# Optimization experiments

Measured on AMD Instinct MI355X. Metric: run time of the kernel, lower is better.

The kernel has to match this reference:

```python
import jax, jax.numpy as jnp
import numpy as np


def _forgetting_attn(q, k, v, g):
    # q, k, v: [B, T, H, D]; g: [B, T, H] per-step log decay (log-space)
    scale = q.shape[-1] ** -0.5
    scores = jnp.einsum('bqhd,bkhd->bhqk', q, k) * scale  # [B,H,T,T]
    gc = jnp.cumsum(g, axis=1).transpose(0, 2, 1)  # [B,H,T]
    scores = scores + gc[:, :, :, None] - gc[:, :, None, :]
    T = q.shape[1]
    causal = jnp.tril(jnp.ones((T, T), dtype=bool))
    scores = jnp.where(causal, scores, -jnp.inf)
    probs = jax.nn.softmax(scores.astype(jnp.float32), axis=-1).astype(q.dtype)
    return jnp.einsum('bhqk,bkhd->bqhd', probs, v)  # [B,T,H,D]


def setup_inputs() -> dict:
    key = jax.random.key(0)
    ks = jax.random.split(key, 7)
    B, T, H = 1, 2048, 1024
    nh = 16
    s = 0.02
    return {
        'hidden_states': jax.random.normal(ks[0], (B, T, H), jnp.float32),
        'Wq': jax.random.normal(ks[1], (H, H), jnp.float32) * s,
        'Wk': jax.random.normal(ks[2], (H, H), jnp.float32) * s,
        'Wv': jax.random.normal(ks[3], (H, H), jnp.float32) * s,
        'Wf': jax.random.normal(ks[4], (nh, H), jnp.float32) * s,
        'bf': jnp.zeros((nh,), jnp.float32),
        'Wo': jax.random.normal(ks[5], (H, 2 * H), jnp.float32) * s,
    }


def reference(hidden_states, Wq, Wk, Wv, Wf, bf, Wo):
    B, T, H = hidden_states.shape
    nh = Wf.shape[0]
    d = H // nh
    q = (hidden_states @ Wq.T).reshape(B, T, nh, d)
    k = (hidden_states @ Wk.T).reshape(B, T, nh, d)
    v = (hidden_states @ Wv.T).reshape(B, T, nh, d)
    f = jax.nn.log_sigmoid((hidden_states @ Wf.T + bf).astype(jnp.float32))  # [B,T,nh]
    o_fwd = _forgetting_attn(q, k, v, f)
    flip = lambda x: jnp.flip(x, axis=1)
    o_bwd = flip(_forgetting_attn(flip(q), flip(k), flip(v), flip(f)))
    o = jnp.concatenate([o_fwd.reshape(B, T, H), o_bwd.reshape(B, T, H)], axis=-1)
    return o @ Wo.T
```

## Files before the change

kernel.cpp:

```cpp
#include <hip/hip_runtime.h>
#include <math.h>

#define T_SEQ 2048
#define HID   1024
#define NH    16
#define HD    64
#define NT    (T_SEQ / 64)

typedef __attribute__((ext_vector_type(8))) __bf16 bf16x8;
typedef __attribute__((ext_vector_type(4))) float  f32x4;
typedef __attribute__((ext_vector_type(8))) unsigned short u16x8;

#define GPTR(p) (const __attribute__((address_space(1))) void*)(p)
#define SPTR(p) (__attribute__((address_space(3))) void*)(p)

__device__ __forceinline__ unsigned short f2bf(float x) {
    unsigned u = __float_as_uint(x);
    u = (u + 0x7FFF + ((u >> 16) & 1)) >> 16;
    return (unsigned short)u;
}
__device__ __forceinline__ float bf2f(unsigned short u) {
    return __uint_as_float((unsigned)u << 16);
}

__global__ __launch_bounds__(256) void prep1(
    const float* __restrict__ hs,
    const float* __restrict__ Wq, const float* __restrict__ Wk,
    const float* __restrict__ Wv, const float* __restrict__ Wo,
    const float* __restrict__ Wf, const float* __restrict__ bfv,
    unsigned short* __restrict__ hsb, unsigned short* __restrict__ wqb,
    unsigned short* __restrict__ wkb, unsigned short* __restrict__ wvb,
    unsigned short* __restrict__ wob, float* __restrict__ f)
{
    const int y = blockIdx.y;
    if (y < 5) {
        const float* in; unsigned short* out; int n;
        switch (y) {
            case 0: in = hs; out = hsb; n = T_SEQ * HID; break;
            case 1: in = Wq; out = wqb; n = HID * HID;   break;
            case 2: in = Wk; out = wkb; n = HID * HID;   break;
            case 3: in = Wv; out = wvb; n = HID * HID;   break;
            default: in = Wo; out = wob; n = HID * 2 * HID; break;
        }
        const int stride = gridDim.x * blockDim.x;
        for (int i = blockIdx.x * blockDim.x + threadIdx.x; i < n / 4; i += stride) {
            float4 v = reinterpret_cast<const float4*>(in)[i];
            ushort4 r;
            r.x = f2bf(v.x); r.y = f2bf(v.y); r.z = f2bf(v.z); r.w = f2bf(v.w);
            reinterpret_cast<ushort4*>(out)[i] = r;
        }
    } else {
        const int t  = blockIdx.x;
        const int h  = threadIdx.x >> 4;
        const int sl = threadIdx.x & 15;
        const float4* hrow = reinterpret_cast<const float4*>(hs + (size_t)t * HID);
        const float4* wrow = reinterpret_cast<const float4*>(Wf + (size_t)h * HID);
        float s = 0.f;
        #pragma unroll
        for (int i = 0; i < 16; ++i) {
            float4 a = hrow[sl + i * 16];
            float4 b = wrow[sl + i * 16];
            s += a.x * b.x + a.y * b.y + a.z * b.z + a.w * b.w;
        }
        s += __shfl_xor(s, 1);
        s += __shfl_xor(s, 2);
        s += __shfl_xor(s, 4);
        s += __shfl_xor(s, 8);
        if (sl == 0) {
            float x = s + bfv[h];
            f[t * NH + h] = (x >= 0.f) ? -log1pf(expf(-x)) : (x - log1pf(expf(x)));
        }
    }
}

template<int NCH, int ROWB>
__device__ __forceinline__ void stage_tile(const unsigned short* __restrict__ G, int K,
                                           int k0, unsigned short* lds, int tid, int w)
{
    #pragma unroll
    for (int j = 0; j < NCH; ++j) {
        const int idxb = j * 4096 + tid * 16;
        const int row  = idxb / ROWB;
        const int kbyt = idxb % ROWB;
        const int col  = (kbyt ^ ((row & 7) << 4)) >> 1;
        const int ldsh = (j * 4096 + w * 1024) >> 1;
        __builtin_amdgcn_global_load_lds(
            GPTR(G + (size_t)row * K + k0 + col), SPTR(lds + ldsh), 16, 0, 0);
    }
}

template<int BM, int BN, int BK, int EMODE>
__global__ __launch_bounds__(256) void gemm_mfma_bt(
    const unsigned short* __restrict__ A,
    const unsigned short* __restrict__ W0, const unsigned short* __restrict__ W1,
    const unsigned short* __restrict__ W2,
    float* __restrict__ C,
    unsigned short* __restrict__ qb, unsigned short* __restrict__ kb,
    unsigned short* __restrict__ vt,
    int M, int N, int K)
{
    const unsigned short* W = blockIdx.z == 0 ? W0 : (blockIdx.z == 1 ? W1 : W2);

    constexpr int FM   = BM / 32;
    constexpr int FN   = BN / 32;
    constexpr int ROWB = BK * 2;
    constexpr int NCHA = BM * BK * 2 / 4096;
    constexpr int NCHB = BN * BK * 2 / 4096;
    constexpr int NKS  = BK / 32;

    __shared__ unsigned short Als[2][BM * BK];
    __shared__ unsigned short Bls[2][BN * BK];

    const int gx  = gridDim.x;
    const int nwg = gx * gridDim.y;
    const int lin = blockIdx.y * gx + blockIdx.x;
    const int cpx = nwg >> 3;
    const int sw  = (lin & 7) * cpx + (lin >> 3);
    const int bx  = sw % gx;
    const int by  = sw / gx;

    const int tid = threadIdx.x;
    const int w   = tid >> 6;
    const int l   = tid & 63;
    const int bm  = by * BM;
    const int bn  = bx * BN;
    const int wm  = (w >> 1) * (BM / 2);
    const int wn  = (w & 1) * (BN / 2);

    f32x4 acc[FM][FN];
    #pragma unroll
    for (int m = 0; m < FM; ++m)
        #pragma unroll
        for (int n = 0; n < FN; ++n) acc[m][n] = (f32x4){0.f, 0.f, 0.f, 0.f};

    const int frow = l & 15;
    const int kgrp = (l >> 4) * 16;
    const int swz  = (l & 7) << 4;

    const unsigned short* Ag = A + (size_t)bm * K;
    const unsigned short* Wg = W + (size_t)bn * K;

    const int NIT = K / BK;
    stage_tile<NCHA, ROWB>(Ag, K, 0, Als[0], tid, w);
    stage_tile<NCHB, ROWB>(Wg, K, 0, Bls[0], tid, w);
    __syncthreads();

    int cur = 0;
    for (int it = 0; it < NIT; ++it) {
        if (it + 1 < NIT) {
            stage_tile<NCHA, ROWB>(Ag, K, (it + 1) * BK, Als[cur ^ 1], tid, w);
            stage_tile<NCHB, ROWB>(Wg, K, (it + 1) * BK, Bls[cur ^ 1], tid, w);
        }
        const unsigned short* Ap = Als[cur];
        const unsigned short* Bp = Bls[cur];
        #pragma unroll
        for (int ks = 0; ks < NKS; ++ks) {
            bf16x8 af[FM], bfr[FN];
            #pragma unroll
            for (int m = 0; m < FM; ++m) {
                const int off = (wm + m * 16 + frow) * ROWB + ((ks * 64 + kgrp) ^ swz);
                af[m] = *reinterpret_cast<const bf16x8*>((const char*)Ap + off);
            }
            #pragma unroll
            for (int n = 0; n < FN; ++n) {
                const int off = (wn + n * 16 + frow) * ROWB + ((ks * 64 + kgrp) ^ swz);
                bfr[n] = *reinterpret_cast<const bf16x8*>((const char*)Bp + off);
            }
            #pragma unroll
            for (int m = 0; m < FM; ++m)
                #pragma unroll
                for (int n = 0; n < FN; ++n)
                    acc[m][n] = __builtin_amdgcn_mfma_f32_16x16x32_bf16(
                        af[m], bfr[n], acc[m][n], 0, 0, 0);
        }
        __syncthreads();
        cur ^= 1;
    }

    const int r0 = (l >> 4) * 4;
    const int cc = l & 15;
    if (EMODE == 1) {
        #pragma unroll
        for (int m = 0; m < FM; ++m)
            #pragma unroll
            for (int n = 0; n < FN; ++n) {
                float* cp = C + (size_t)(bm + wm + m * 16 + r0) * N + bn + wn + n * 16 + cc;
                #pragma unroll
                for (int r = 0; r < 4; ++r) cp[(size_t)r * N] = acc[m][n][r];
            }
    } else {
        const int z = blockIdx.z;
        if (z == 0) {
            #pragma unroll
            for (int m = 0; m < FM; ++m) {
                const int t0 = bm + wm + m * 16 + r0;
                #pragma unroll
                for (int n = 0; n < FN; ++n) {
                    const int col = bn + wn + n * 16 + cc;
                    #pragma unroll
                    for (int r = 0; r < 4; ++r)
                        qb[(size_t)(t0 + r) * HID + col] = f2bf(acc[m][n][r] * 0.125f);
                }
            }
        } else if (z == 1) {
            #pragma unroll
            for (int m = 0; m < FM; ++m) {
                const int t0 = bm + wm + m * 16 + r0;
                #pragma unroll
                for (int n = 0; n < FN; ++n) {
                    const int col = bn + wn + n * 16 + cc;
                    const int hh  = col >> 6;
                    const int d   = col & 63;
                    #pragma unroll
                    for (int r = 0; r < 4; ++r)
                        kb[(size_t)hh * T_SEQ * HD + (size_t)(t0 + r) * HD + d] =
                            f2bf(acc[m][n][r]);
                }
            }
        } else {
            #pragma unroll
            for (int m = 0; m < FM; ++m) {
                const int t0 = bm + wm + m * 16 + r0;
                #pragma unroll
                for (int n = 0; n < FN; ++n) {
                    const int col = bn + wn + n * 16 + cc;
                    const int hh  = col >> 6;
                    const int d   = col & 63;
                    ushort4 pk;
                    pk.x = f2bf(acc[m][n][0]); pk.y = f2bf(acc[m][n][1]);
                    pk.z = f2bf(acc[m][n][2]); pk.w = f2bf(acc[m][n][3]);
                    *reinterpret_cast<ushort4*>(
                        vt + (size_t)hh * HD * T_SEQ + (size_t)d * T_SEQ + t0) = pk;
                }
            }
        }
    }
}

__global__ __launch_bounds__(256) void prep2(const float* __restrict__ f,
                                             float* __restrict__ gcf,
                                             float* __restrict__ gcb,
                                             const unsigned short* __restrict__ kb,
                                             float* __restrict__ knmax)
{
    const int bid = blockIdx.x;
    if (bid < 32) {
        const int h   = bid >> 1;
        const int rev = bid & 1;
        float* out = rev ? gcb : gcf;
        const int wv   = threadIdx.x >> 6;
        const int lane = threadIdx.x & 63;
        __shared__ float wtot[4];
        float vals[8];
        float run = 0.f;
        #pragma unroll
        for (int c = 0; c < 8; ++c) {
            const int p = wv * 512 + c * 64 + lane;
            const int t = rev ? (T_SEQ - 1 - p) : p;
            float x = f[t * NH + h];
            #pragma unroll
            for (int off = 1; off < 64; off <<= 1) {
                float y = __shfl_up(x, off);
                if (lane >= off) x += y;
            }
            vals[c] = run + x;
            run += __shfl(x, 63);
        }
        if (lane == 0) wtot[wv] = run;
        __syncthreads();
        float prefix = 0.f;
        #pragma unroll
        for (int i = 0; i < 4; ++i) prefix += (i < wv) ? wtot[i] : 0.f;
        #pragma unroll
        for (int c = 0; c < 8; ++c) {
            const int p = wv * 512 + c * 64 + lane;
            const int t = rev ? (T_SEQ - 1 - p) : p;
            out[t * NH + h] = vals[c] + prefix;
        }
    } else {
        const int h    = bid - 32;
        const int tid  = threadIdx.x;
        const int wv   = tid >> 6;
        const int lane = tid & 63;
        __shared__ float wmax[4];
        float mx = 0.f;
        for (int t = tid; t < T_SEQ; t += 256) {
            const u16x8* kr = reinterpret_cast<const u16x8*>(
                kb + (size_t)h * T_SEQ * HD + (size_t)t * HD);
            float s = 0.f;
            #pragma unroll
            for (int i = 0; i < 8; ++i) {
                u16x8 v8 = kr[i];
                #pragma unroll
                for (int j = 0; j < 8; ++j) { float x = bf2f(v8[j]); s += x * x; }
            }
            mx = fmaxf(mx, s);
        }
        #pragma unroll
        for (int off = 32; off > 0; off >>= 1) mx = fmaxf(mx, __shfl_xor(mx, off));
        if (lane == 0) wmax[wv] = mx;
        __syncthreads();
        if (tid == 0) {
            float m = fmaxf(fmaxf(wmax[0], wmax[1]), fmaxf(wmax[2], wmax[3]));
            knmax[h] = sqrtf(m);
        }
    }
}

__global__ __launch_bounds__(256) void attn_flash(
    const unsigned short* __restrict__ qb, const unsigned short* __restrict__ kg,
    const unsigned short* __restrict__ vg,
    const float* __restrict__ gcf, const float* __restrict__ gcb,
    const float* __restrict__ knmax,
    unsigned short* __restrict__ ocat)
{
    const int dir = blockIdx.z;
    const float* gc = dir ? gcb : gcf;
    const int h   = blockIdx.y;
    const int qt  = blockIdx.x;
    const int q0  = qt * 64;
    const int tid = threadIdx.x;
    const int w   = tid >> 6;
    const int l   = tid & 63;
    const int lm  = l & 15;
    const int lg  = l >> 4;
    const int swz = (l & 7) << 4;

    __shared__ unsigned short Kls[64 * 64];
    __shared__ unsigned short Vls[64 * 64];
    __shared__ unsigned short Pls[64 * 64];
    __shared__ float gks[64];
    __shared__ float qbs[64];

    const size_t kgbase = (size_t)h * T_SEQ * HD;
    const size_t vgbase = (size_t)h * HD * T_SEQ;

    const int qrow_a = q0 + 16 * w + lm;
    bf16x8 aq[2];
    aq[0] = *reinterpret_cast<const bf16x8*>(qb + (size_t)qrow_a * HID + h * HD + lg * 8);
    aq[1] = *reinterpret_cast<const bf16x8*>(qb + (size_t)qrow_a * HID + h * HD + 32 + lg * 8);
    float qn2 = 0.f;
    #pragma unroll
    for (int ks = 0; ks < 2; ++ks) {
        u16x8 uv = *reinterpret_cast<const u16x8*>(&aq[ks]);
        #pragma unroll
        for (int j = 0; j < 8; ++j) { float x = bf2f(uv[j]); qn2 += x * x; }
    }
    qn2 += __shfl_xor(qn2, 16);
    qn2 += __shfl_xor(qn2, 32);
    if (lg == 0) qbs[16 * w + lm] = sqrtf(qn2) * knmax[h];

    float gq_r[4];
    #pragma unroll
    for (int reg = 0; reg < 4; ++reg)
        gq_r[reg] = gc[(q0 + 16 * w + lg * 4 + reg) * NH + h];

    float mrun[4], lrun[4];
    #pragma unroll
    for (int reg = 0; reg < 4; ++reg) { mrun[reg] = -1e30f; lrun[reg] = 0.f; }
    f32x4 acc[4];
    #pragma unroll
    for (int db = 0; db < 4; ++db) acc[db] = (f32x4){0.f, 0.f, 0.f, 0.f};

    const int stp = dir ? 1 : -1;
    for (int kt = qt; kt >= 0 && kt < NT; kt += stp) {
        const int k0 = kt * 64;

        #pragma unroll
        for (int j = 0; j < 2; ++j) {
            const int idxb = j * 4096 + tid * 16;
            const int row  = idxb >> 7;
            const int kbyt = idxb & 127;
            const int scol = (kbyt ^ ((row & 7) << 4)) >> 1;
            const int ldsh = (j * 4096 + w * 1024) >> 1;
            __builtin_amdgcn_global_load_lds(
                GPTR(kg + kgbase + (size_t)(k0 + row) * HD + scol),
                SPTR(Kls + ldsh), 16, 0, 0);
            __builtin_amdgcn_global_load_lds(
                GPTR(vg + vgbase + (size_t)row * T_SEQ + k0 + scol),
                SPTR(Vls + ldsh), 16, 0, 0);
        }
        if (w == 0)
            __builtin_amdgcn_global_load_lds(
                GPTR(gc + (size_t)(k0 + l) * NH + h), SPTR(gks), 4, 0, 0);
        __syncthreads();

        f32x4 s[4];
        #pragma unroll
        for (int cb = 0; cb < 4; ++cb) {
            bf16x8 b0 = *reinterpret_cast<const bf16x8*>(
                (char*)Kls + (cb * 16 + lm) * 128 + ((lg * 16) ^ swz));
            bf16x8 b1 = *reinterpret_cast<const bf16x8*>(
                (char*)Kls + (cb * 16 + lm) * 128 + ((64 + lg * 16) ^ swz));
            f32x4 z = (f32x4){0.f, 0.f, 0.f, 0.f};
            z = __builtin_amdgcn_mfma_f32_16x16x32_bf16(aq[0], b0, z, 0, 0, 0);
            s[cb] = __builtin_amdgcn_mfma_f32_16x16x32_bf16(aq[1], b1, z, 0, 0, 0);
        }

        float gk_c[4];
        #pragma unroll
        for (int cb = 0; cb < 4; ++cb) gk_c[cb] = gks[cb * 16 + lm];
        float sv[4][4];
        const bool diag = (kt == qt);
        #pragma unroll
        for (int cb = 0; cb < 4; ++cb)
            #pragma unroll
            for (int reg = 0; reg < 4; ++reg) {
                float x = s[cb][reg] + gq_r[reg] - gk_c[cb];
                if (diag) {
                    const int c_loc = cb * 16 + lm;
                    const int r_loc = 16 * w + lg * 4 + reg;
                    const bool valid = dir ? (c_loc >= r_loc) : (c_loc <= r_loc);
                    x = valid ? x : -1e30f;
                }
                sv[cb][reg] = x;
            }

        float corr[4], mnew[4];
        #pragma unroll
        for (int reg = 0; reg < 4; ++reg) {
            float rm = fmaxf(fmaxf(sv[0][reg], sv[1][reg]), fmaxf(sv[2][reg], sv[3][reg]));
            rm = fmaxf(rm, __shfl_xor(rm, 1));
            rm = fmaxf(rm, __shfl_xor(rm, 2));
            rm = fmaxf(rm, __shfl_xor(rm, 4));
            rm = fmaxf(rm, __shfl_xor(rm, 8));
            mnew[reg] = fmaxf(mrun[reg], rm);
            corr[reg] = __expf(mrun[reg] - mnew[reg]);
            mrun[reg] = mnew[reg];
        }
        float psum[4] = {0.f, 0.f, 0.f, 0.f};
        #pragma unroll
        for (int cb = 0; cb < 4; ++cb)
            #pragma unroll
            for (int reg = 0; reg < 4; ++reg) {
                const float p = __expf(sv[cb][reg] - mnew[reg]);
                psum[reg] += p;
                const int r_loc = 16 * w + lg * 4 + reg;
                *reinterpret_cast<unsigned short*>(
                    (char*)Pls + r_loc * 128 + ((cb * 32 + lm * 2) ^ ((r_loc & 7) << 4))) = f2bf(p);
            }
        #pragma unroll
        for (int reg = 0; reg < 4; ++reg) {
            float ps = psum[reg];
            ps += __shfl_xor(ps, 1);
            ps += __shfl_xor(ps, 2);
            ps += __shfl_xor(ps, 4);
            ps += __shfl_xor(ps, 8);
            lrun[reg] = lrun[reg] * corr[reg] + ps;
        }
        #pragma unroll
        for (int db = 0; db < 4; ++db)
            #pragma unroll
            for (int reg = 0; reg < 4; ++reg) acc[db][reg] *= corr[reg];

        bf16x8 ap[2];
        #pragma unroll
        for (int ks = 0; ks < 2; ++ks)
            ap[ks] = *reinterpret_cast<const bf16x8*>(
                (char*)Pls + (16 * w + lm) * 128 + ((ks * 64 + lg * 16) ^ swz));
        #pragma unroll
        for (int db = 0; db < 4; ++db) {
            bf16x8 bv0 = *reinterpret_cast<const bf16x8*>(
                (char*)Vls + (db * 16 + lm) * 128 + ((lg * 16) ^ swz));
            bf16x8 bv1 = *reinterpret_cast<const bf16x8*>(
                (char*)Vls + (db * 16 + lm) * 128 + ((64 + lg * 16) ^ swz));
            acc[db] = __builtin_amdgcn_mfma_f32_16x16x32_bf16(ap[0], bv0, acc[db], 0, 0, 0);
            acc[db] = __builtin_amdgcn_mfma_f32_16x16x32_bf16(ap[1], bv1, acc[db], 0, 0, 0);
        }

        const int nkt = kt + stp;
        if (nkt >= 0 && nkt < NT) {
            const float gkedge = dir ? gc[(nkt * 64) * NH + h]
                                     : gc[(nkt * 64 + 63) * NH + h];
            int pred = 0;
            #pragma unroll
            for (int reg = 0; reg < 4; ++reg) {
                const float qbv = qbs[16 * w + lg * 4 + reg];
                pred |= (qbv + gq_r[reg] - gkedge) >= (mrun[reg] - 15.f);
            }
            if (!__syncthreads_or(pred)) break;
        }
    }

    float inv[4];
    #pragma unroll
    for (int reg = 0; reg < 4; ++reg) inv[reg] = 1.f / lrun[reg];
    #pragma unroll
    for (int db = 0; db < 4; ++db)
        #pragma unroll
        for (int reg = 0; reg < 4; ++reg) {
            const int row = q0 + 16 * w + lg * 4 + reg;
            const int col = db * 16 + lm;
            ocat[(size_t)row * (2 * HID) + dir * HID + h * HD + col] =
                f2bf(acc[db][reg] * inv[reg]);
        }
}

extern "C" void kernel_launch(void* const* d_in, const int* in_sizes, int n_in,
                              void* d_out, int out_size, void* d_ws, size_t ws_size,
                              hipStream_t stream)
{
    (void)in_sizes; (void)n_in; (void)out_size; (void)ws_size;
    const float* hs = (const float*)d_in[0];
    const float* Wq = (const float*)d_in[1];
    const float* Wk = (const float*)d_in[2];
    const float* Wv = (const float*)d_in[3];
    const float* Wf = (const float*)d_in[4];
    const float* bf = (const float*)d_in[5];
    const float* Wo = (const float*)d_in[6];
    float* out = (float*)d_out;

    float* ws    = (float*)d_ws;
    float* f     = ws;
    float* gcf   = f   + (size_t)T_SEQ * NH;
    float* gcb   = gcf + (size_t)T_SEQ * NH;
    float* knmax = gcb + (size_t)T_SEQ * NH;
    unsigned short* hsb  = (unsigned short*)(knmax + 64);
    unsigned short* wqb  = hsb + (size_t)T_SEQ * HID;
    unsigned short* wkb  = wqb + (size_t)HID * HID;
    unsigned short* wvb  = wkb + (size_t)HID * HID;
    unsigned short* wob  = wvb + (size_t)HID * HID;
    unsigned short* qb   = wob + (size_t)HID * 2 * HID;
    unsigned short* kb   = qb  + (size_t)T_SEQ * HID;
    unsigned short* vt   = kb  + (size_t)T_SEQ * HID;
    unsigned short* ocat = vt  + (size_t)T_SEQ * HID;

    prep1<<<dim3(2048, 6), 256, 0, stream>>>(
        hs, Wq, Wk, Wv, Wo, Wf, bf, hsb, wqb, wkb, wvb, wob, f);

    gemm_mfma_bt<128, 64, 64, 0><<<dim3(HID / 64, T_SEQ / 128, 3), 256, 0, stream>>>(
        hsb, wqb, wkb, wvb, nullptr, qb, kb, vt, T_SEQ, HID, HID);

    prep2<<<48, 256, 0, stream>>>(f, gcf, gcb, kb, knmax);

    attn_flash<<<dim3(NT, NH, 2), 256, 0, stream>>>(qb, kb, vt, gcf, gcb, knmax, ocat);

    gemm_mfma_bt<64, 64, 128, 1><<<dim3(HID / 64, T_SEQ / 64, 1), 256, 0, stream>>>(
        ocat, wob, nullptr, nullptr, out, nullptr, nullptr, nullptr,
        T_SEQ, HID, 2 * HID);
}
```

Measured before the change: 89.11 us.

## Fuse Q/K/V projections into one GEMM sharing the activation tile

```diff
diff --git a/kernel.cpp b/kernel.cpp
--- a/kernel.cpp
+++ b/kernel.cpp
@@ -89,27 +89,16 @@
     }
 }
 
-template<int BM, int BN, int BK, int EMODE>
-__global__ __launch_bounds__(256) void gemm_mfma_bt(
+__global__ __launch_bounds__(256) void gemm_qkv(
     const unsigned short* __restrict__ A,
-    const unsigned short* __restrict__ W0, const unsigned short* __restrict__ W1,
-    const unsigned short* __restrict__ W2,
-    float* __restrict__ C,
+    const unsigned short* __restrict__ Wq_, const unsigned short* __restrict__ Wk_,
+    const unsigned short* __restrict__ Wv_,
     unsigned short* __restrict__ qb, unsigned short* __restrict__ kb,
-    unsigned short* __restrict__ vt,
-    int M, int N, int K)
-{
-    const unsigned short* W = blockIdx.z == 0 ? W0 : (blockIdx.z == 1 ? W1 : W2);
-
-    constexpr int FM   = BM / 32;
-    constexpr int FN   = BN / 32;
-    constexpr int ROWB = BK * 2;
-    constexpr int NCHA = BM * BK * 2 / 4096;
-    constexpr int NCHB = BN * BK * 2 / 4096;
-    constexpr int NKS  = BK / 32;
-
-    __shared__ unsigned short Als[2][BM * BK];
-    __shared__ unsigned short Bls[2][BN * BK];
+    unsigned short* __restrict__ vt)
+{
+    constexpr int K = HID;
+    __shared__ unsigned short Als[2][128 * 64];
+    __shared__ unsigned short Bls[3][2][64 * 64];
 
     const int gx  = gridDim.x;
     const int nwg = gx * gridDim.y;
@@ -122,6 +111,121 @@
     const int tid = threadIdx.x;
     const int w   = tid >> 6;
     const int l   = tid & 63;
+    const int bm  = by * 128;
+    const int hh  = bx;
+    const int wm  = (w >> 1) * 64;
+    const int wn  = (w & 1) * 32;
+
+    f32x4 acc[3][4][2];
+    #pragma unroll
+    for (int z = 0; z < 3; ++z)
+        #pragma unroll
+        for (int m = 0; m < 4; ++m)
+            #pragma unroll
+            for (int n = 0; n < 2; ++n) acc[z][m][n] = (f32x4){0.f, 0.f, 0.f, 0.f};
+
+    const int frow = l & 15;
+    const int kgrp = (l >> 4) * 16;
+    const int swz  = (l & 7) << 4;
+
+    const unsigned short* Ag  = A   + (size_t)bm * K;
+    const unsigned short* Wgq = Wq_ + (size_t)hh * 64 * K;
+    const unsigned short* Wgk = Wk_ + (size_t)hh * 64 * K;
+    const unsigned short* Wgv = Wv_ + (size_t)hh * 64 * K;
+
+    stage_tile<4, 128>(Ag,  K, 0, Als[0],    tid, w);
+    stage_tile<2, 128>(Wgq, K, 0, Bls[0][0], tid, w);
+    stage_tile<2, 128>(Wgk, K, 0, Bls[1][0], tid, w);
+    stage_tile<2, 128>(Wgv, K, 0, Bls[2][0], tid, w);
+    __syncthreads();
+
+    int cur = 0;
+    for (int it = 0; it < K / 64; ++it) {
+        if (it + 1 < K / 64) {
+            const int k1 = (it + 1) * 64;
+            stage_tile<4, 128>(Ag,  K, k1, Als[cur ^ 1],    tid, w);
+            stage_tile<2, 128>(Wgq, K, k1, Bls[0][cur ^ 1], tid, w);
+            stage_tile<2, 128>(Wgk, K, k1, Bls[1][cur ^ 1], tid, w);
+            stage_tile<2, 128>(Wgv, K, k1, Bls[2][cur ^ 1], tid, w);
+        }
+        #pragma unroll
+        for (int ks = 0; ks < 2; ++ks) {
+            bf16x8 af[4];
+            #pragma unroll
+            for (int m = 0; m < 4; ++m) {
+                const int off = (wm + m * 16 + frow) * 128 + ((ks * 64 + kgrp) ^ swz);
+                af[m] = *reinterpret_cast<const bf16x8*>((const char*)Als[cur] + off);
+            }
+            #pragma unroll
+            for (int z = 0; z < 3; ++z) {
+                bf16x8 bfr[2];
+                #pragma unroll
+                for (int n = 0; n < 2; ++n) {
+                    const int off = (wn + n * 16 + frow) * 128 + ((ks * 64 + kgrp) ^ swz);
+                    bfr[n] = *reinterpret_cast<const bf16x8*>((const char*)Bls[z][cur] + off);
+                }
+                #pragma unroll
+                for (int m = 0; m < 4; ++m)
+                    #pragma unroll
+                    for (int n = 0; n < 2; ++n)
+                        acc[z][m][n] = __builtin_amdgcn_mfma_f32_16x16x32_bf16(
+                            af[m], bfr[n], acc[z][m][n], 0, 0, 0);
+            }
+        }
+        __syncthreads();
+        cur ^= 1;
+    }
+
+    const int r0 = (l >> 4) * 4;
+    const int cc = l & 15;
+    #pragma unroll
+    for (int m = 0; m < 4; ++m) {
+        const int t0 = bm + wm + m * 16 + r0;
+        #pragma unroll
+        for (int n = 0; n < 2; ++n) {
+            const int d   = wn + n * 16 + cc;
+            const int col = hh * 64 + d;
+            #pragma unroll
+            for (int r = 0; r < 4; ++r) {
+                qb[(size_t)(t0 + r) * HID + col] = f2bf(acc[0][m][n][r] * 0.125f);
+                kb[(size_t)hh * T_SEQ * HD + (size_t)(t0 + r) * HD + d] =
+                    f2bf(acc[1][m][n][r]);
+            }
+            ushort4 pk;
+            pk.x = f2bf(acc[2][m][n][0]); pk.y = f2bf(acc[2][m][n][1]);
+            pk.z = f2bf(acc[2][m][n][2]); pk.w = f2bf(acc[2][m][n][3]);
+            *reinterpret_cast<ushort4*>(
+                vt + (size_t)hh * HD * T_SEQ + (size_t)d * T_SEQ + t0) = pk;
+        }
+    }
+}
+
+template<int BM, int BN, int BK>
+__global__ __launch_bounds__(256) void gemm_out(
+    const unsigned short* __restrict__ A, const unsigned short* __restrict__ W,
+    float* __restrict__ C, int M, int N, int K)
+{
+    constexpr int FM   = BM / 32;
+    constexpr int FN   = BN / 32;
+    constexpr int ROWB = BK * 2;
+    constexpr int NCHA = BM * BK * 2 / 4096;
+    constexpr int NCHB = BN * BK * 2 / 4096;
+    constexpr int NKS  = BK / 32;
+
+    __shared__ unsigned short Als[2][BM * BK];
+    __shared__ unsigned short Bls[2][BN * BK];
+
+    const int gx  = gridDim.x;
+    const int nwg = gx * gridDim.y;
+    const int lin = blockIdx.y * gx + blockIdx.x;
+    const int cpx = nwg >> 3;
+    const int sw  = (lin & 7) * cpx + (lin >> 3);
+    const int bx  = sw % gx;
+    const int by  = sw / gx;
+
+    const int tid = threadIdx.x;
+    const int w   = tid >> 6;
+    const int l   = tid & 63;
     const int bm  = by * BM;
     const int bn  = bx * BN;
     const int wm  = (w >> 1) * (BM / 2);
@@ -179,62 +283,14 @@
 
     const int r0 = (l >> 4) * 4;
     const int cc = l & 15;
-    if (EMODE == 1) {
-        #pragma unroll
-        for (int m = 0; m < FM; ++m)
-            #pragma unroll
-            for (int n = 0; n < FN; ++n) {
-                float* cp = C + (size_t)(bm + wm + m * 16 + r0) * N + bn + wn + n * 16 + cc;
-                #pragma unroll
-                for (int r = 0; r < 4; ++r) cp[(size_t)r * N] = acc[m][n][r];
-            }
-    } else {
-        const int z = blockIdx.z;
-        if (z == 0) {
-            #pragma unroll
-            for (int m = 0; m < FM; ++m) {
-                const int t0 = bm + wm + m * 16 + r0;
-                #pragma unroll
-                for (int n = 0; n < FN; ++n) {
-                    const int col = bn + wn + n * 16 + cc;
-                    #pragma unroll
-                    for (int r = 0; r < 4; ++r)
-                        qb[(size_t)(t0 + r) * HID + col] = f2bf(acc[m][n][r] * 0.125f);
-                }
-            }
-        } else if (z == 1) {
-            #pragma unroll
-            for (int m = 0; m < FM; ++m) {
-                const int t0 = bm + wm + m * 16 + r0;
-                #pragma unroll
-                for (int n = 0; n < FN; ++n) {
-                    const int col = bn + wn + n * 16 + cc;
-                    const int hh  = col >> 6;
-                    const int d   = col & 63;
-                    #pragma unroll
-                    for (int r = 0; r < 4; ++r)
-                        kb[(size_t)hh * T_SEQ * HD + (size_t)(t0 + r) * HD + d] =
-                            f2bf(acc[m][n][r]);
-                }
-            }
-        } else {
-            #pragma unroll
-            for (int m = 0; m < FM; ++m) {
-                const int t0 = bm + wm + m * 16 + r0;
-                #pragma unroll
-                for (int n = 0; n < FN; ++n) {
-                    const int col = bn + wn + n * 16 + cc;
-                    const int hh  = col >> 6;
-                    const int d   = col & 63;
-                    ushort4 pk;
-                    pk.x = f2bf(acc[m][n][0]); pk.y = f2bf(acc[m][n][1]);
-                    pk.z = f2bf(acc[m][n][2]); pk.w = f2bf(acc[m][n][3]);
-                    *reinterpret_cast<ushort4*>(
-                        vt + (size_t)hh * HD * T_SEQ + (size_t)d * T_SEQ + t0) = pk;
-                }
-            }
-        }
-    }
+    #pragma unroll
+    for (int m = 0; m < FM; ++m)
+        #pragma unroll
+        for (int n = 0; n < FN; ++n) {
+            float* cp = C + (size_t)(bm + wm + m * 16 + r0) * N + bn + wn + n * 16 + cc;
+            #pragma unroll
+            for (int r = 0; r < 4; ++r) cp[(size_t)r * N] = acc[m][n][r];
+        }
 }
 
 __global__ __launch_bounds__(256) void prep2(const float* __restrict__ f,
@@ -528,14 +584,13 @@
     prep1<<<dim3(2048, 6), 256, 0, stream>>>(
         hs, Wq, Wk, Wv, Wo, Wf, bf, hsb, wqb, wkb, wvb, wob, f);
 
-    gemm_mfma_bt<128, 64, 64, 0><<<dim3(HID / 64, T_SEQ / 128, 3), 256, 0, stream>>>(
-        hsb, wqb, wkb, wvb, nullptr, qb, kb, vt, T_SEQ, HID, HID);
+    gemm_qkv<<<dim3(NH, T_SEQ / 128), 256, 0, stream>>>(
+        hsb, wqb, wkb, wvb, qb, kb, vt);
 
     prep2<<<48, 256, 0, stream>>>(f, gcf, gcb, kb, knmax);
 
     attn_flash<<<dim3(NT, NH, 2), 256, 0, stream>>>(qb, kb, vt, gcf, gcb, knmax, ocat);
 
-    gemm_mfma_bt<64, 64, 128, 1><<<dim3(HID / 64, T_SEQ / 64, 1), 256, 0, stream>>>(
-        ocat, wob, nullptr, nullptr, out, nullptr, nullptr, nullptr,
-        T_SEQ, HID, 2 * HID);
-}
+    gemm_out<64, 64, 128><<<dim3(HID / 64, T_SEQ / 64), 256, 0, stream>>>(
+        ocat, wob, out, T_SEQ, HID, 2 * HID);
+}
```

New measurement: 100.2 us. 12.4% more time.
